# Kernel optimization log

Hardware: AMD Instinct MI355X
Metric: run time of the kernel (lower is better)

The kernel has to match this reference:

```python
import jax, jax.numpy as jnp
import numpy as np
from functools import partial

NUM_CLASSES = 4
HEAD_OUTS = [4, 2, 1, 3, 2, 2]  # class, offset, z, size, yaw, vel -> sum 14
VOXEL = (0.1, 0.1)
PC_RANGE = (0.0, -39.68, -3.0, 100.0, 39.68, 1.0)
MIN_RADIUS = 2.0
BN_EPS = 1e-5


def setup_inputs() -> dict:
    key = jax.random.key(0)
    ks = jax.random.split(key, 12)
    B, C, H, W, N = 4, 256, 200, 200, 128
    spatial_features = jax.random.normal(ks[0], (B, C, H, W), jnp.float32)
    # gt boxes: x,y,z,w,l,h,yaw,cls,vx,vy ; coords chosen so grid idx in [0,200)
    x = jax.random.uniform(ks[1], (B, N), jnp.float32, 0.5, 19.5)
    y = jax.random.uniform(ks[2], (B, N), jnp.float32, -39.0, -20.0)
    z = jax.random.uniform(ks[3], (B, N), jnp.float32, -2.0, 0.0)
    dims = jax.random.uniform(ks[4], (B, N, 3), jnp.float32, 1.0, 4.0)
    yaw = jax.random.uniform(ks[5], (B, N), jnp.float32, -3.14159, 3.14159)
    cls = jax.random.randint(ks[6], (B, N), 0, NUM_CLASSES).astype(jnp.float32)
    vel = 0.1 * jax.random.normal(ks[7], (B, N, 2), jnp.float32)
    gt = jnp.concatenate([x[..., None], y[..., None], z[..., None], dims,
                          yaw[..., None], cls[..., None], vel], axis=-1)
    # zero out last 16 boxes per sample -> filtered by validity mask
    gt = gt.at[:, -16:, :].set(0.0)
    w1 = 0.05 * jax.random.normal(ks[8], (6, C, C, 3, 3), jnp.float32)
    bn_gamma = jnp.ones((6, C), jnp.float32)
    bn_beta = jnp.zeros((6, C), jnp.float32)
    bn_mean = 0.1 * jax.random.normal(ks[9], (6, C), jnp.float32)
    bn_var = jax.random.uniform(ks[10], (6, C), jnp.float32, 0.5, 1.5)
    w2 = 0.05 * jax.random.normal(ks[11], (14, C, 1, 1), jnp.float32)
    b2 = jnp.zeros((14,), jnp.float32)
    return {"spatial_features": spatial_features, "gt_boxes": gt, "w1": w1,
            "bn_gamma": bn_gamma, "bn_beta": bn_beta, "bn_mean": bn_mean,
            "bn_var": bn_var, "w2": w2, "b2": b2}


def _conv(x, w, pad):
    return jax.lax.conv_general_dilated(x, w, (1, 1), pad,
                                        dimension_numbers=("NCHW", "OIHW", "NCHW"))


def _heads(x, w1, g, b, m, v, w2, b2):
    outs, o = [], 0
    for i, nout in enumerate(HEAD_OUTS):
        h = _conv(x, w1[i], "SAME")  # [B,C,H,W]
        h = g[i][None, :, None, None] * (h - m[i][None, :, None, None]) \
            * jax.lax.rsqrt(v[i][None, :, None, None] + BN_EPS) + b[i][None, :, None, None]
        h = jax.nn.relu(h)
        outs.append(_conv(h, w2[o:o + nout], "VALID") + b2[o:o + nout][None, :, None, None])
        o += nout
    return jnp.concatenate(outs, axis=1)  # [B,14,H,W]


def _targets(gt, H, W):
    B, N = gt.shape[:2]
    x, y, z = gt[..., 0], gt[..., 1], gt[..., 2]
    bw, bl, bh = gt[..., 3], gt[..., 4], gt[..., 5]
    yaw = gt[..., 6]
    cls = jnp.clip(gt[..., 7].astype(jnp.int32), 0, NUM_CLASSES - 1)
    vel = gt[..., 8:10]
    valid = (jnp.abs(x) + jnp.abs(y) + jnp.abs(z)) > 0
    gx = (x - PC_RANGE[0]) / VOXEL[0]
    gy = (y - PC_RANGE[1]) / VOXEL[1]
    gxi = jnp.floor(gx).astype(jnp.int32)
    gyi = jnp.floor(gy).astype(jnp.int32)
    valid = valid & (gxi >= 0) & (gxi < W) & (gyi >= 0) & (gyi < H)
    xoff = gx - gxi.astype(gx.dtype)
    yoff = gy - gyi.astype(gy.dtype)
    # scalar targets scatter (invalid boxes dropped via out-of-range flat index)
    vals = jnp.stack([xoff, yoff, z, bw, bl, bh, jnp.sin(yaw), jnp.cos(yaw),
                      vel[..., 0], vel[..., 1], jnp.ones_like(x)], axis=-1)  # [B,N,11]
    bidx = jnp.broadcast_to(jnp.arange(B, dtype=jnp.int32)[:, None], (B, N))
    flat = bidx * (H * W) + gyi * W + gxi
    flat = jnp.where(valid, flat, B * H * W)  # out of range -> dropped
    scat = jnp.zeros((B * H * W, 11), jnp.float32)
    scat = scat.at[flat.reshape(-1)].set(vals.reshape(-1, 11), mode="drop")
    scalars = scat.reshape(B, H, W, 11).transpose(0, 3, 1, 2)  # [B,11,H,W]
    # gaussian heatmap: per-box splat, scatter-max into class channel
    sigma = jnp.maximum(jnp.sqrt(bw ** 2 + bl ** 2) / 2.0, MIN_RADIUS) / 3.0  # [B,N]
    xs = jnp.arange(W, dtype=jnp.float32)
    ys = jnp.arange(H, dtype=jnp.float32)
    d2 = (xs[None, None, None, :] - gxi[..., None, None].astype(jnp.float32)) ** 2 + \
         (ys[None, None, :, None] - gyi[..., None, None].astype(jnp.float32)) ** 2  # [B,N,H,W]
    gauss = jnp.exp(-d2 / (2.0 * sigma[..., None, None] ** 2))
    gauss = jnp.where(valid[..., None, None], gauss, 0.0)
    heat = jnp.zeros((B, NUM_CLASSES, H, W), jnp.float32)
    heat = heat.at[bidx, cls].max(gauss)
    return jnp.concatenate([heat, scalars], axis=1)  # [B,15,H,W]


def reference(spatial_features, gt_boxes, w1, bn_gamma, bn_beta, bn_mean, bn_var, w2, b2):
    H, W = spatial_features.shape[-2:]
    preds = _heads(spatial_features, w1, bn_gamma, bn_beta, bn_mean, bn_var, w2, b2)
    tgts = _targets(gt_boxes, H, W)
    return jnp.concatenate([preds, tgts], axis=1)  # [B,29,H,W]
```

## Files before the change

kernel.cpp:

```cpp
#include <hip/hip_runtime.h>

typedef __attribute__((ext_vector_type(8))) short short8;
typedef __attribute__((ext_vector_type(4))) float f32x4;
typedef __attribute__((ext_vector_type(4))) unsigned short us4;
typedef __attribute__((ext_vector_type(8))) unsigned short us8;

union FragU { short8 s; us4 h[2]; us8 u; };

__device__ __forceinline__ unsigned short f2bf(float f) {
  union { float f; unsigned int u; } v; v.f = f;
  unsigned int r = (v.u + 0x7fffu + ((v.u >> 16) & 1u)) >> 16;
  return (unsigned short)r;
}

__global__ void transpose_k(const float* __restrict__ sf, unsigned short* __restrict__ Xt) {
  __shared__ float tile[32][33];
  int b = blockIdx.z, c0 = blockIdx.y * 32, p0 = blockIdx.x * 32;
  int tx = threadIdx.x, ty = threadIdx.y;
#pragma unroll
  for (int i = 0; i < 4; ++i)
    tile[ty + i * 8][tx] = sf[((size_t)(b * 256 + c0 + ty + i * 8) * 40000) + p0 + tx];
  __syncthreads();
#pragma unroll
  for (int i = 0; i < 4; ++i)
    Xt[((size_t)(b * 40000 + p0 + ty + i * 8) << 8) + c0 + tx] = f2bf(tile[tx][ty + i * 8]);
}

__global__ void prep_w1f_k(const float* __restrict__ w1, const float* __restrict__ gamma,
                           const float* __restrict__ var, unsigned short* __restrict__ W1f) {
  int id = blockIdx.x * 256 + threadIdx.x;
  if (id >= 6 * 256 * 2304) return;
  int k = id % 2304;
  int rest = id / 2304;
  int oc = rest & 255, h = rest >> 8;
  int tap = k >> 8, c = k & 255;
  int hc = h * 256 + oc;
  float s = gamma[hc] * rsqrtf(var[hc] + 1e-5f);
  W1f[id] = f2bf(s * w1[(hc * 256 + c) * 9 + tap]);
}

__global__ __launch_bounds__(512) void conv_head_xt_k(
    const unsigned short* __restrict__ Xt, const unsigned short* __restrict__ W1f,
    const float* __restrict__ gamma, const float* __restrict__ beta,
    const float* __restrict__ mean, const float* __restrict__ var,
    const float* __restrict__ w2, const float* __restrict__ b2,
    float* __restrict__ out) {
  const int NOUT[6] = {4, 2, 1, 3, 2, 2};
  const int OFFS[6] = {0, 4, 6, 7, 10, 12};
  __shared__ __align__(16) char smem[78080];
  unsigned short* A_s  = (unsigned short*)smem;
  unsigned short* B_s  = (unsigned short*)(smem + 9216);
  unsigned short* h_s  = (unsigned short*)smem;
  unsigned short* w2_s = (unsigned short*)(smem + 67584);
  float* tb_s          = (float*)(smem + 76032);

  int tid = threadIdx.x;
  int head = blockIdx.z, b = blockIdx.y;
  int p_loc = blockIdx.x * 128;
  int nout = NOUT[head], ooff = OFFS[head];

  {
    int j = tid >> 5, c8 = (tid & 31) * 8;
    us8 t;
#pragma unroll
    for (int q = 0; q < 8; ++q)
      t[q] = (j < nout) ? f2bf(w2[(ooff + j) * 256 + c8 + q]) : (unsigned short)0;
    *(us8*)&w2_s[j * 264 + c8] = t;
  }
  if (tid < 256) {
    int hc = head * 256 + tid;
    float s = gamma[hc] * rsqrtf(var[hc] + 1e-5f);
    tb_s[tid] = beta[hc] - s * mean[hc];
  }
  __syncthreads();

  int wid = tid >> 6, lane = tid & 63;
  int wm = wid >> 2, wn = wid & 3;
  int l15 = lane & 15, lhi = lane >> 4;

  int apx = tid >> 2, cofs = (tid & 3) << 3;
  int pA = p_loc + apx;
  int aay = pA / 200, aax = pA - aay * 200;
  const unsigned short* xb = Xt + ((size_t)b * 40000 << 8);

  int oc = tid >> 1, half = tid & 1;
  const unsigned short* wsrc = W1f + (size_t)(head * 256 + oc) * 2304 + half * 16;

  f32x4 acc[4][4];
#pragma unroll
  for (int mi = 0; mi < 4; ++mi)
#pragma unroll
    for (int ni = 0; ni < 4; ++ni) acc[mi][ni] = (f32x4){0.f, 0.f, 0.f, 0.f};

  us8 aN, b0N, b1N;
  {
    int yy = aay - 1, xx = aax - 1;
    aN = (us8){0, 0, 0, 0, 0, 0, 0, 0};
    if ((unsigned)yy < 200u && (unsigned)xx < 200u)
      aN = *(const us8*)&xb[((size_t)(yy * 200 + xx) << 8) + cofs];
    b0N = *(const us8*)(wsrc);
    b1N = *(const us8*)(wsrc + 8);
  }

  for (int kt = 0; kt < 72; ++kt) {
    {
      FragU ua; ua.u = aN;
      int ao = apx * 36 + cofs;
      *(us4*)&A_s[ao] = ua.h[0];
      *(us4*)&A_s[ao + 4] = ua.h[1];
      FragU u0, u1; u0.u = b0N; u1.u = b1N;
      int bo = oc * 36 + half * 16;
      *(us4*)&B_s[bo]      = u0.h[0];
      *(us4*)&B_s[bo + 4]  = u0.h[1];
      *(us4*)&B_s[bo + 8]  = u1.h[0];
      *(us4*)&B_s[bo + 12] = u1.h[1];
    }
    __syncthreads();

    if (kt < 71) {
      int kn = kt + 1;
      int tap = kn >> 3, c0 = (kn & 7) << 5;
      int t3 = tap / 3;
      int dy = t3 - 1, dx = tap - t3 * 3 - 1;
      int yy = aay + dy, xx = aax + dx;
      aN = (us8){0, 0, 0, 0, 0, 0, 0, 0};
      if ((unsigned)yy < 200u && (unsigned)xx < 200u)
        aN = *(const us8*)&xb[((size_t)(yy * 200 + xx) << 8) + c0 + cofs];
      b0N = *(const us8*)(wsrc + kn * 32);
      b1N = *(const us8*)(wsrc + kn * 32 + 8);
    }

    short8 af[4], bfr[4];
#pragma unroll
    for (int mi = 0; mi < 4; ++mi) {
      int a = (wm * 64 + mi * 16 + l15) * 36 + lhi * 8;
      FragU u;
      u.h[0] = *(const us4*)&A_s[a];
      u.h[1] = *(const us4*)&A_s[a + 4];
      af[mi] = u.s;
    }
#pragma unroll
    for (int ni = 0; ni < 4; ++ni) {
      int a = (wn * 64 + ni * 16 + l15) * 36 + lhi * 8;
      FragU u;
      u.h[0] = *(const us4*)&B_s[a];
      u.h[1] = *(const us4*)&B_s[a + 4];
      bfr[ni] = u.s;
    }
#pragma unroll
    for (int mi = 0; mi < 4; ++mi)
#pragma unroll
      for (int ni = 0; ni < 4; ++ni)
        acc[mi][ni] = __builtin_amdgcn_mfma_f32_16x16x32_bf16(af[mi], bfr[ni], acc[mi][ni], 0, 0, 0);
    __syncthreads();
  }

#pragma unroll
  for (int mi = 0; mi < 4; ++mi) {
#pragma unroll
    for (int ni = 0; ni < 4; ++ni) {
      int ocl = wn * 64 + ni * 16 + l15;
      float tbv = tb_s[ocl];
#pragma unroll
      for (int r = 0; r < 4; ++r) {
        int px = wm * 64 + mi * 16 + lhi * 4 + r;
        float v = fmaxf(acc[mi][ni][r] + tbv, 0.f);
        h_s[px * 264 + ocl] = f2bf(v);
      }
    }
  }
  __syncthreads();

  {
    int j = l15;
    float b2v = (j < nout) ? b2[ooff + j] : 0.f;
    f32x4 oacc = (f32x4){0.f, 0.f, 0.f, 0.f};
#pragma unroll
    for (int kc = 0; kc < 8; ++kc) {
      int koff = kc * 32 + lhi * 8;
      FragU hu, wu;
      hu.u = *(const us8*)&h_s[(wid * 16 + l15) * 264 + koff];
      wu.u = *(const us8*)&w2_s[l15 * 264 + koff];
      oacc = __builtin_amdgcn_mfma_f32_16x16x32_bf16(hu.s, wu.s, oacc, 0, 0, 0);
    }
    if (j < nout) {
      float* dst = out + (size_t)(b * 29 + ooff + j) * 40000;
#pragma unroll
      for (int r = 0; r < 4; ++r) {
        int px_g = p_loc + wid * 16 + lhi * 4 + r;
        if (px_g < 40000) dst[px_g] = oacc[r] + b2v;
      }
    }
  }
}

template <int BMODE>
__global__ __launch_bounds__(512) void conv_head_mfma_k(
    const float* __restrict__ sf, const unsigned short* __restrict__ W1f,
    const float* __restrict__ w1, const float* __restrict__ gamma,
    const float* __restrict__ beta, const float* __restrict__ mean,
    const float* __restrict__ var, const float* __restrict__ w2,
    const float* __restrict__ b2, float* __restrict__ out) {
  const int NOUT[6] = {4, 2, 1, 3, 2, 2};
  const int OFFS[6] = {0, 4, 6, 7, 10, 12};
  __shared__ __align__(16) char smem[78080];
  unsigned short* A_s  = (unsigned short*)smem;
  unsigned short* B_s  = (unsigned short*)(smem + 9216);
  unsigned short* h_s  = (unsigned short*)smem;
  unsigned short* w2_s = (unsigned short*)(smem + 67584);
  float* tb_s          = (float*)(smem + 76032);
  float* s_s           = (float*)(smem + 77056);

  int tid = threadIdx.x;
  int head = blockIdx.z, b = blockIdx.y;
  int p_loc = blockIdx.x * 128;
  int nout = NOUT[head], ooff = OFFS[head];
  {
    int j = tid >> 5, c8 = (tid & 31) * 8;
    us8 t;
#pragma unroll
    for (int q = 0; q < 8; ++q)
      t[q] = (j < nout) ? f2bf(w2[(ooff + j) * 256 + c8 + q]) : (unsigned short)0;
    *(us8*)&w2_s[j * 264 + c8] = t;
  }
  if (tid < 256) {
    int hc = head * 256 + tid;
    float s = gamma[hc] * rsqrtf(var[hc] + 1e-5f);
    s_s[tid] = s;
    tb_s[tid] = beta[hc] - s * mean[hc];
  }
  __syncthreads();

  int wid = tid >> 6, lane = tid & 63;
  int wm = wid >> 2, wn = wid & 3;
  int l15 = lane & 15, lhi = lane >> 4;
  int cg = wid, mm = lane;
  int p0 = p_loc + mm, p1 = p0 + 64;
  int ay0 = p0 / 200, ax0 = p0 - ay0 * 200;
  int ay1 = p1 / 200, ax1 = p1 - ay1 * 200;
  const float* sfb = sf + (size_t)b * 256 * 40000;
  int oc = tid >> 1, half = tid & 1;
  const unsigned short* wsrc = W1f + (size_t)(head * 256 + oc) * 2304 + half * 16;
  const float* w1h = w1 + ((size_t)head * 256 + oc) * 2304;
  float sv = s_s[oc];

  f32x4 acc[4][4];
#pragma unroll
  for (int mi = 0; mi < 4; ++mi)
#pragma unroll
    for (int ni = 0; ni < 4; ++ni) acc[mi][ni] = (f32x4){0.f, 0.f, 0.f, 0.f};

  for (int kt = 0; kt < 72; ++kt) {
    int tap = kt >> 3;
    int c0 = (kt & 7) << 5;
    int t3 = tap / 3;
    int dy = t3 - 1, dx = tap - t3 * 3 - 1;
    {
      const float* src = sfb + (size_t)(c0 + cg * 4) * 40000;
      int yy = ay0 + dy, xx = ax0 + dx;
      us4 v = (us4){0, 0, 0, 0};
      if ((unsigned)yy < 200u && (unsigned)xx < 200u) {
        int pix = yy * 200 + xx;
        v[0] = f2bf(src[pix]);
        v[1] = f2bf(src[40000 + pix]);
        v[2] = f2bf(src[80000 + pix]);
        v[3] = f2bf(src[120000 + pix]);
      }
      *(us4*)&A_s[mm * 36 + cg * 4] = v;
      yy = ay1 + dy; xx = ax1 + dx;
      us4 w = (us4){0, 0, 0, 0};
      if ((unsigned)yy < 200u && (unsigned)xx < 200u) {
        int pix = yy * 200 + xx;
        w[0] = f2bf(src[pix]);
        w[1] = f2bf(src[40000 + pix]);
        w[2] = f2bf(src[80000 + pix]);
        w[3] = f2bf(src[120000 + pix]);
      }
      *(us4*)&A_s[(mm + 64) * 36 + cg * 4] = w;
    }
    if (BMODE == 0) {
      FragU u0, u1;
      u0.u = *(const us8*)(wsrc + kt * 32);
      u1.u = *(const us8*)(wsrc + kt * 32 + 8);
      int bo = oc * 36 + half * 16;
      *(us4*)&B_s[bo]      = u0.h[0];
      *(us4*)&B_s[bo + 4]  = u0.h[1];
      *(us4*)&B_s[bo + 8]  = u1.h[0];
      *(us4*)&B_s[bo + 12] = u1.h[1];
    } else {
      int kk = half * 16;
#pragma unroll
      for (int g = 0; g < 4; ++g) {
        us4 t;
#pragma unroll
        for (int q = 0; q < 4; ++q)
          t[q] = f2bf(sv * w1h[(c0 + kk + g * 4 + q) * 9 + tap]);
        *(us4*)&B_s[oc * 36 + kk + g * 4] = t;
      }
    }
    __syncthreads();
    short8 af[4], bfr[4];
#pragma unroll
    for (int mi = 0; mi < 4; ++mi) {
      int a = (wm * 64 + mi * 16 + l15) * 36 + lhi * 8;
      FragU u;
      u.h[0] = *(const us4*)&A_s[a];
      u.h[1] = *(const us4*)&A_s[a + 4];
      af[mi] = u.s;
    }
#pragma unroll
    for (int ni = 0; ni < 4; ++ni) {
      int a = (wn * 64 + ni * 16 + l15) * 36 + lhi * 8;
      FragU u;
      u.h[0] = *(const us4*)&B_s[a];
      u.h[1] = *(const us4*)&B_s[a + 4];
      bfr[ni] = u.s;
    }
#pragma unroll
    for (int mi = 0; mi < 4; ++mi)
#pragma unroll
      for (int ni = 0; ni < 4; ++ni)
        acc[mi][ni] = __builtin_amdgcn_mfma_f32_16x16x32_bf16(af[mi], bfr[ni], acc[mi][ni], 0, 0, 0);
    __syncthreads();
  }
#pragma unroll
  for (int mi = 0; mi < 4; ++mi) {
#pragma unroll
    for (int ni = 0; ni < 4; ++ni) {
      int ocl = wn * 64 + ni * 16 + l15;
      float tbv = tb_s[ocl];
#pragma unroll
      for (int r = 0; r < 4; ++r) {
        int px = wm * 64 + mi * 16 + lhi * 4 + r;
        float v = fmaxf(acc[mi][ni][r] + tbv, 0.f);
        h_s[px * 264 + ocl] = f2bf(v);
      }
    }
  }
  __syncthreads();
  {
    int j = l15;
    float b2v = (j < nout) ? b2[ooff + j] : 0.f;
    f32x4 oacc = (f32x4){0.f, 0.f, 0.f, 0.f};
#pragma unroll
    for (int kc = 0; kc < 8; ++kc) {
      int koff = kc * 32 + lhi * 8;
      FragU hu, wu;
      hu.u = *(const us8*)&h_s[(wid * 16 + l15) * 264 + koff];
      wu.u = *(const us8*)&w2_s[l15 * 264 + koff];
      oacc = __builtin_amdgcn_mfma_f32_16x16x32_bf16(hu.s, wu.s, oacc, 0, 0, 0);
    }
    if (j < nout) {
      float* dst = out + (size_t)(b * 29 + ooff + j) * 40000;
#pragma unroll
      for (int r = 0; r < 4; ++r) {
        int px_g = p_loc + wid * 16 + lhi * 4 + r;
        if (px_g < 40000) dst[px_g] = oacc[r] + b2v;
      }
    }
  }
}

__global__ void heat_k(const float* __restrict__ gt, float* __restrict__ out) {
  __shared__ float bx[128], by[128], binv[128];
  __shared__ int bcls[128];
  int b = blockIdx.y, tid = threadIdx.x;
  if (tid < 128) {
    const float* g = gt + (b * 128 + tid) * 10;
    float x = g[0], y = g[1], z = g[2];
    bool valid = fabsf(x) + fabsf(y) + fabsf(z) > 0.f;
    float gx = x / 0.1f;
    float gy = (y + 39.68f) / 0.1f;
    float fx = floorf(gx), fy = floorf(gy);
    int gxi = (int)fx, gyi = (int)fy;
    valid = valid && gxi >= 0 && gxi < 200 && gyi >= 0 && gyi < 200;
    float bw = g[3], bl = g[4];
    float sigma = fmaxf(sqrtf(bw * bw + bl * bl) * 0.5f, 2.0f) / 3.0f;
    binv[tid] = valid ? 1.f / (2.f * sigma * sigma) : -1.f;
    bx[tid] = fx;
    by[tid] = fy;
    bcls[tid] = min(max((int)g[7], 0), 3);
  }
  __syncthreads();
  int pid = blockIdx.x * 256 + tid;
  if (pid >= 40000) return;
  float py = (float)(pid / 200);
  float px = (float)(pid - (pid / 200) * 200);
  float h0 = 0.f, h1 = 0.f, h2 = 0.f, h3 = 0.f;
  for (int n = 0; n < 128; ++n) {
    float inv = binv[n];
    if (inv < 0.f) continue;
    float ddx = px - bx[n], ddy = py - by[n];
    float t = (ddx * ddx + ddy * ddy) * inv;
    if (t > 40.f) continue;
    float e = __expf(-t);
    int c = bcls[n];
    h0 = fmaxf(h0, c == 0 ? e : 0.f);
    h1 = fmaxf(h1, c == 1 ? e : 0.f);
    h2 = fmaxf(h2, c == 2 ? e : 0.f);
    h3 = fmaxf(h3, c == 3 ? e : 0.f);
  }
  int base = (b * 29 + 14) * 40000 + pid;
  out[base] = h0;
  out[base + 40000] = h1;
  out[base + 80000] = h2;
  out[base + 120000] = h3;
#pragma unroll
  for (int q = 0; q < 11; ++q) out[base + (4 + q) * 40000] = 0.f;
}

__global__ void scatter_k(const float* __restrict__ gt, float* __restrict__ out) {
  int b = threadIdx.x;
  if (b >= 4) return;
  for (int n = 0; n < 128; ++n) {
    const float* g = gt + (b * 128 + n) * 10;
    float x = g[0], y = g[1], z = g[2];
    if (!(fabsf(x) + fabsf(y) + fabsf(z) > 0.f)) continue;
    float gx = x / 0.1f;
    float gy = (y + 39.68f) / 0.1f;
    float fx = floorf(gx), fy = floorf(gy);
    int gxi = (int)fx, gyi = (int)fy;
    if (gxi < 0 || gxi >= 200 || gyi < 0 || gyi >= 200) continue;
    int base = (b * 29 + 18) * 40000 + gyi * 200 + gxi;
    out[base] = gx - fx;
    out[base + 1 * 40000] = gy - fy;
    out[base + 2 * 40000] = z;
    out[base + 3 * 40000] = g[3];
    out[base + 4 * 40000] = g[4];
    out[base + 5 * 40000] = g[5];
    out[base + 6 * 40000] = sinf(g[6]);
    out[base + 7 * 40000] = cosf(g[6]);
    out[base + 8 * 40000] = g[8];
    out[base + 9 * 40000] = g[9];
    out[base + 10 * 40000] = 1.f;
  }
}

extern "C" void kernel_launch(void* const* d_in, const int* in_sizes, int n_in,
                              void* d_out, int out_size, void* d_ws, size_t ws_size,
                              hipStream_t stream) {
  const float* sf    = (const float*)d_in[0];
  const float* gt    = (const float*)d_in[1];
  const float* w1    = (const float*)d_in[2];
  const float* gamma = (const float*)d_in[3];
  const float* beta  = (const float*)d_in[4];
  const float* mean  = (const float*)d_in[5];
  const float* var   = (const float*)d_in[6];
  const float* w2    = (const float*)d_in[7];
  const float* b2    = (const float*)d_in[8];
  float* out = (float*)d_out;
  char* ws = (char*)d_ws;

  const size_t W1F_BYTES = (size_t)6 * 256 * 2304 * 2;
  const size_t XT_BYTES  = (size_t)4 * 40000 * 256 * 2;
  unsigned short* W1f = (unsigned short*)ws;
  unsigned short* Xt  = (unsigned short*)(ws + W1F_BYTES);

  dim3 cgrid(313, 4, 6);
  if (ws_size >= W1F_BYTES + XT_BYTES) {
    prep_w1f_k<<<(6 * 256 * 2304 + 255) / 256, 256, 0, stream>>>(w1, gamma, var, W1f);
    transpose_k<<<dim3(1250, 8, 4), dim3(32, 8), 0, stream>>>(sf, Xt);
    conv_head_xt_k<<<cgrid, 512, 0, stream>>>(Xt, W1f, gamma, beta, mean, var, w2, b2, out);
  } else if (ws_size >= W1F_BYTES) {
    prep_w1f_k<<<(6 * 256 * 2304 + 255) / 256, 256, 0, stream>>>(w1, gamma, var, W1f);
    conv_head_mfma_k<0><<<cgrid, 512, 0, stream>>>(sf, W1f, w1, gamma, beta, mean, var, w2, b2, out);
  } else {
    conv_head_mfma_k<1><<<cgrid, 512, 0, stream>>>(sf, (const unsigned short*)nullptr,
                                                   w1, gamma, beta, mean, var, w2, b2, out);
  }
  heat_k<<<dim3(157, 4), 256, 0, stream>>>(gt, out);
  scatter_k<<<1, 64, 0, stream>>>(gt, out);
}
```

Measured before the change: 1.373 ms.

## Add padded-halo input layout and double-buffered direct-to-LDS loads in conv head

Adds a transpose kernel that writes bf16 activations into a zero-padded (202x202) pixel-major buffer. The new conv kernel can then load im2col tiles with no bounds checks, using global_load_lds so data goes straight from global memory into double-buffered LDS. This removes the register round-trip and the second barrier each K-step, and overlaps the next tile's load with the MFMA work. In exchange it needs a larger workspace and a full memset of the padded buffer each call, and it drops the old LDS row padding, which risks bank conflicts.

After: 1.277 ms. 7.0% less time.

```diff
diff --git a/kernel.cpp b/kernel.cpp
--- a/kernel.cpp
+++ b/kernel.cpp
@@ -11,6 +11,29 @@
   union { float f; unsigned int u; } v; v.f = f;
   unsigned int r = (v.u + 0x7fffu + ((v.u >> 16) & 1u)) >> 16;
   return (unsigned short)r;
+}
+
+typedef const __attribute__((address_space(1))) unsigned int* gas1_t;
+typedef __attribute__((address_space(3))) unsigned int* las3_t;
+__device__ __forceinline__ void glds16(const void* g, void* l) {
+  __builtin_amdgcn_global_load_lds((gas1_t)g, (las3_t)l, 16, 0, 0);
+}
+
+__global__ void transpose_pad_k(const float* __restrict__ sf, unsigned short* __restrict__ Xtp) {
+  __shared__ float tile[32][33];
+  int b = blockIdx.z, c0 = blockIdx.y * 32, p0 = blockIdx.x * 32;
+  int tx = threadIdx.x, ty = threadIdx.y;
+#pragma unroll
+  for (int i = 0; i < 4; ++i)
+    tile[ty + i * 8][tx] = sf[((size_t)(b * 256 + c0 + ty + i * 8) * 40000) + p0 + tx];
+  __syncthreads();
+#pragma unroll
+  for (int i = 0; i < 4; ++i) {
+    int p = p0 + ty + i * 8;
+    int y = p / 200, x = p - y * 200;
+    size_t pf = (size_t)b * 40804 + (size_t)(y + 1) * 202 + (x + 1);
+    Xtp[(pf << 8) + c0 + tx] = f2bf(tile[tx][ty + i * 8]);
+  }
 }
 
 __global__ void transpose_k(const float* __restrict__ sf, unsigned short* __restrict__ Xt) {
@@ -37,6 +60,140 @@
   int hc = h * 256 + oc;
   float s = gamma[hc] * rsqrtf(var[hc] + 1e-5f);
   W1f[id] = f2bf(s * w1[(hc * 256 + c) * 9 + tap]);
+}
+
+__global__ __launch_bounds__(512) void conv_head_glds_k(
+    const unsigned short* __restrict__ Xtp, const unsigned short* __restrict__ W1f,
+    const float* __restrict__ gamma, const float* __restrict__ beta,
+    const float* __restrict__ mean, const float* __restrict__ var,
+    const float* __restrict__ w2, const float* __restrict__ b2,
+    float* __restrict__ out) {
+  const int NOUT[6] = {4, 2, 1, 3, 2, 2};
+  const int OFFS[6] = {0, 4, 6, 7, 10, 12};
+  __shared__ __align__(16) char smem[77056];
+  unsigned short* h_s  = (unsigned short*)smem;
+  unsigned short* w2_s = (unsigned short*)(smem + 67584);
+  float* tb_s          = (float*)(smem + 76032);
+
+  int tid = threadIdx.x;
+  int head = blockIdx.z, b = blockIdx.y;
+  int p_loc = blockIdx.x * 128;
+  int nout = NOUT[head], ooff = OFFS[head];
+
+  {
+    int j = tid >> 5, c8 = (tid & 31) * 8;
+    us8 t;
+#pragma unroll
+    for (int q = 0; q < 8; ++q)
+      t[q] = (j < nout) ? f2bf(w2[(ooff + j) * 256 + c8 + q]) : (unsigned short)0;
+    *(us8*)&w2_s[j * 264 + c8] = t;
+  }
+  if (tid < 256) {
+    int hc = head * 256 + tid;
+    float s = gamma[hc] * rsqrtf(var[hc] + 1e-5f);
+    tb_s[tid] = beta[hc] - s * mean[hc];
+  }
+
+  int wid = tid >> 6, lane = tid & 63;
+  int wm = wid >> 2, wn = wid & 3;
+  int l15 = lane & 15, lhi = lane >> 4;
+
+  int apx = tid >> 2, cofs = (tid & 3) << 3;
+  int pA = p_loc + apx;
+  int pAc = pA < 40000 ? pA : 39999;
+  int ayy = pAc / 200, axx = pAc - ayy * 200;
+  int aflat = (ayy + 1) * 202 + (axx + 1);
+  const unsigned short* xbp = Xtp + (((size_t)b * 40804) << 8);
+
+  const unsigned short* bG0 = W1f + (size_t)(head * 256 + wid * 32 + (lane >> 2)) * 2304 + (lane & 3) * 8;
+  const unsigned short* bG1 = bG0 + 16 * 2304;
+
+  char* AL[2] = {smem + wid * 1024, smem + 24576 + wid * 1024};
+  char* BL[2] = {smem + 8192 + wid * 2048, smem + 32768 + wid * 2048};
+
+  f32x4 acc[4][4];
+#pragma unroll
+  for (int mi = 0; mi < 4; ++mi)
+#pragma unroll
+    for (int ni = 0; ni < 4; ++ni) acc[mi][ni] = (f32x4){0.f, 0.f, 0.f, 0.f};
+
+  glds16(xbp + (((size_t)(aflat - 203)) << 8) + cofs, AL[0]);
+  glds16(bG0, BL[0]);
+  glds16(bG1, BL[0] + 1024);
+  __syncthreads();
+
+  for (int kt = 0; kt < 72; ++kt) {
+    int cur = kt & 1;
+    if (kt < 71) {
+      int kn = kt + 1;
+      int tap = kn >> 3, c0 = (kn & 7) << 5;
+      int t3 = tap / 3;
+      int doff = (t3 - 1) * 202 + (tap - t3 * 3 - 1);
+      glds16(xbp + (((size_t)(aflat + doff)) << 8) + c0 + cofs, AL[cur ^ 1]);
+      glds16(bG0 + kn * 32, BL[cur ^ 1]);
+      glds16(bG1 + kn * 32, BL[cur ^ 1] + 1024);
+    }
+
+    const unsigned short* A_sh = (const unsigned short*)(smem + (cur ? 24576 : 0));
+    const unsigned short* B_sh = (const unsigned short*)(smem + (cur ? 32768 : 8192));
+    short8 af[4], bfr[4];
+#pragma unroll
+    for (int mi = 0; mi < 4; ++mi) {
+      FragU u;
+      u.u = *(const us8*)&A_sh[(wm * 64 + mi * 16 + l15) * 32 + lhi * 8];
+      af[mi] = u.s;
+    }
+#pragma unroll
+    for (int ni = 0; ni < 4; ++ni) {
+      FragU u;
+      u.u = *(const us8*)&B_sh[(wn * 64 + ni * 16 + l15) * 32 + lhi * 8];
+      bfr[ni] = u.s;
+    }
+#pragma unroll
+    for (int mi = 0; mi < 4; ++mi)
+#pragma unroll
+      for (int ni = 0; ni < 4; ++ni)
+        acc[mi][ni] = __builtin_amdgcn_mfma_f32_16x16x32_bf16(af[mi], bfr[ni], acc[mi][ni], 0, 0, 0);
+    __syncthreads();
+  }
+
+#pragma unroll
+  for (int mi = 0; mi < 4; ++mi) {
+#pragma unroll
+    for (int ni = 0; ni < 4; ++ni) {
+      int ocl = wn * 64 + ni * 16 + l15;
+      float tbv = tb_s[ocl];
+#pragma unroll
+      for (int r = 0; r < 4; ++r) {
+        int px = wm * 64 + mi * 16 + lhi * 4 + r;
+        float v = fmaxf(acc[mi][ni][r] + tbv, 0.f);
+        h_s[px * 264 + ocl] = f2bf(v);
+      }
+    }
+  }
+  __syncthreads();
+
+  {
+    int j = l15;
+    float b2v = (j < nout) ? b2[ooff + j] : 0.f;
+    f32x4 oacc = (f32x4){0.f, 0.f, 0.f, 0.f};
+#pragma unroll
+    for (int kc = 0; kc < 8; ++kc) {
+      int koff = kc * 32 + lhi * 8;
+      FragU hu, wu;
+      hu.u = *(const us8*)&h_s[(wid * 16 + l15) * 264 + koff];
+      wu.u = *(const us8*)&w2_s[l15 * 264 + koff];
+      oacc = __builtin_amdgcn_mfma_f32_16x16x32_bf16(hu.s, wu.s, oacc, 0, 0, 0);
+    }
+    if (j < nout) {
+      float* dst = out + (size_t)(b * 29 + ooff + j) * 40000;
+#pragma unroll
+      for (int r = 0; r < 4; ++r) {
+        int px_g = p_loc + wid * 16 + lhi * 4 + r;
+        if (px_g < 40000) dst[px_g] = oacc[r] + b2v;
+      }
+    }
+  }
 }
 
 __global__ __launch_bounds__(512) void conv_head_xt_k(
@@ -58,7 +215,6 @@
   int head = blockIdx.z, b = blockIdx.y;
   int p_loc = blockIdx.x * 128;
   int nout = NOUT[head], ooff = OFFS[head];
-
   {
     int j = tid >> 5, c8 = (tid & 31) * 8;
     us8 t;
@@ -77,12 +233,10 @@
   int wid = tid >> 6, lane = tid & 63;
   int wm = wid >> 2, wn = wid & 3;
   int l15 = lane & 15, lhi = lane >> 4;
-
   int apx = tid >> 2, cofs = (tid & 3) << 3;
   int pA = p_loc + apx;
   int aay = pA / 200, aax = pA - aay * 200;
   const unsigned short* xb = Xt + ((size_t)b * 40000 << 8);
-
   int oc = tid >> 1, half = tid & 1;
   const unsigned short* wsrc = W1f + (size_t)(head * 256 + oc) * 2304 + half * 16;
 
@@ -116,7 +270,6 @@
       *(us4*)&B_s[bo + 12] = u1.h[1];
     }
     __syncthreads();
-
     if (kt < 71) {
       int kn = kt + 1;
       int tap = kn >> 3, c0 = (kn & 7) << 5;
@@ -129,7 +282,6 @@
       b0N = *(const us8*)(wsrc + kn * 32);
       b1N = *(const us8*)(wsrc + kn * 32 + 8);
     }
-
     short8 af[4], bfr[4];
 #pragma unroll
     for (int mi = 0; mi < 4; ++mi) {
@@ -154,7 +306,6 @@
         acc[mi][ni] = __builtin_amdgcn_mfma_f32_16x16x32_bf16(af[mi], bfr[ni], acc[mi][ni], 0, 0, 0);
     __syncthreads();
   }
-
 #pragma unroll
   for (int mi = 0; mi < 4; ++mi) {
 #pragma unroll
@@ -170,7 +321,6 @@
     }
   }
   __syncthreads();
-
   {
     int j = l15;
     float b2v = (j < nout) ? b2[ooff + j] : 0.f;
@@ -194,13 +344,12 @@
   }
 }
 
-template <int BMODE>
-__global__ __launch_bounds__(512) void conv_head_mfma_k(
-    const float* __restrict__ sf, const unsigned short* __restrict__ W1f,
-    const float* __restrict__ w1, const float* __restrict__ gamma,
-    const float* __restrict__ beta, const float* __restrict__ mean,
-    const float* __restrict__ var, const float* __restrict__ w2,
-    const float* __restrict__ b2, float* __restrict__ out) {
+__global__ __launch_bounds__(512) void conv_head_nows_k(
+    const float* __restrict__ sf, const float* __restrict__ w1,
+    const float* __restrict__ gamma, const float* __restrict__ beta,
+    const float* __restrict__ mean, const float* __restrict__ var,
+    const float* __restrict__ w2, const float* __restrict__ b2,
+    float* __restrict__ out) {
   const int NOUT[6] = {4, 2, 1, 3, 2, 2};
   const int OFFS[6] = {0, 4, 6, 7, 10, 12};
   __shared__ __align__(16) char smem[78080];
@@ -240,7 +389,6 @@
   int ay1 = p1 / 200, ax1 = p1 - ay1 * 200;
   const float* sfb = sf + (size_t)b * 256 * 40000;
   int oc = tid >> 1, half = tid & 1;
-  const unsigned short* wsrc = W1f + (size_t)(head * 256 + oc) * 2304 + half * 16;
   const float* w1h = w1 + ((size_t)head * 256 + oc) * 2304;
   float sv = s_s[oc];
 
@@ -278,16 +426,7 @@
       }
       *(us4*)&A_s[(mm + 64) * 36 + cg * 4] = w;
     }
-    if (BMODE == 0) {
-      FragU u0, u1;
-      u0.u = *(const us8*)(wsrc + kt * 32);
-      u1.u = *(const us8*)(wsrc + kt * 32 + 8);
-      int bo = oc * 36 + half * 16;
-      *(us4*)&B_s[bo]      = u0.h[0];
-      *(us4*)&B_s[bo + 4]  = u0.h[1];
-      *(us4*)&B_s[bo + 8]  = u1.h[0];
-      *(us4*)&B_s[bo + 12] = u1.h[1];
-    } else {
+    {
       int kk = half * 16;
 #pragma unroll
       for (int g = 0; g < 4; ++g) {
@@ -453,20 +592,23 @@
 
   const size_t W1F_BYTES = (size_t)6 * 256 * 2304 * 2;
   const size_t XT_BYTES  = (size_t)4 * 40000 * 256 * 2;
+  const size_t XTP_BYTES = (size_t)4 * 40804 * 256 * 2;
   unsigned short* W1f = (unsigned short*)ws;
-  unsigned short* Xt  = (unsigned short*)(ws + W1F_BYTES);
 
   dim3 cgrid(313, 4, 6);
-  if (ws_size >= W1F_BYTES + XT_BYTES) {
+  if (ws_size >= W1F_BYTES + XTP_BYTES) {
+    unsigned short* Xtp = (unsigned short*)(ws + W1F_BYTES);
+    prep_w1f_k<<<(6 * 256 * 2304 + 255) / 256, 256, 0, stream>>>(w1, gamma, var, W1f);
+    hipMemsetAsync(Xtp, 0, XTP_BYTES, stream);
+    transpose_pad_k<<<dim3(1250, 8, 4), dim3(32, 8), 0, stream>>>(sf, Xtp);
+    conv_head_glds_k<<<cgrid, 512, 0, stream>>>(Xtp, W1f, gamma, beta, mean, var, w2, b2, out);
+  } else if (ws_size >= W1F_BYTES + XT_BYTES) {
+    unsigned short* Xt = (unsigned short*)(ws + W1F_BYTES);
     prep_w1f_k<<<(6 * 256 * 2304 + 255) / 256, 256, 0, stream>>>(w1, gamma, var, W1f);
     transpose_k<<<dim3(1250, 8, 4), dim3(32, 8), 0, stream>>>(sf, Xt);
     conv_head_xt_k<<<cgrid, 512, 0, stream>>>(Xt, W1f, gamma, beta, mean, var, w2, b2, out);
-  } else if (ws_size >= W1F_BYTES) {
-    prep_w1f_k<<<(6 * 256 * 2304 + 255) / 256, 256, 0, stream>>>(w1, gamma, var, W1f);
-    conv_head_mfma_k<0><<<cgrid, 512, 0, stream>>>(sf, W1f, w1, gamma, beta, mean, var, w2, b2, out);
   } else {
-    conv_head_mfma_k<1><<<cgrid, 512, 0, stream>>>(sf, (const unsigned short*)nullptr,
-                                                   w1, gamma, beta, mean, var, w2, b2, out);
+    conv_head_nows_k<<<cgrid, 512, 0, stream>>>(sf, w1, gamma, beta, mean, var, w2, b2, out);
   }
   heat_k<<<dim3(157, 4), 256, 0, stream>>>(gt, out);
   scatter_k<<<1, 64, 0, stream>>>(gt, out);
```

## Use zero-padded NHWC input and double-buffered direct-to-LDS loads in conv heads

Applied to the files above, without the earlier changes.

The transpose now writes into a zero-padded 202x202 bf16 NHWC buffer, so the conv kernel no longer needs boundary checks. The new conv kernel uses 256 threads with a 4x8 MFMA tile per wave and global_load_lds to copy A and B tiles straight into double-buffered shared memory, overlapping the next K-step's loads with the current MFMAs. The aim is to remove register staging, the extra barrier and the branchy loads. In exchange it adds a memset of the padded buffer, needs more accumulator registers, and drops the weight-only fallback path.

New measurement: 1.293 ms. 5.8% less time.

```diff
diff --git a/kernel.cpp b/kernel.cpp
--- a/kernel.cpp
+++ b/kernel.cpp
@@ -13,7 +13,13 @@
   return (unsigned short)r;
 }
 
-__global__ void transpose_k(const float* __restrict__ sf, unsigned short* __restrict__ Xt) {
+typedef const __attribute__((address_space(1))) unsigned int* gas1_t;
+typedef __attribute__((address_space(3))) unsigned int* las3_t;
+__device__ __forceinline__ void glds16(const void* g, void* l) {
+  __builtin_amdgcn_global_load_lds((gas1_t)g, (las3_t)l, 16, 0, 0);
+}
+
+__global__ void transpose_pad_k(const float* __restrict__ sf, unsigned short* __restrict__ Xtp) {
   __shared__ float tile[32][33];
   int b = blockIdx.z, c0 = blockIdx.y * 32, p0 = blockIdx.x * 32;
   int tx = threadIdx.x, ty = threadIdx.y;
@@ -22,8 +28,12 @@
     tile[ty + i * 8][tx] = sf[((size_t)(b * 256 + c0 + ty + i * 8) * 40000) + p0 + tx];
   __syncthreads();
 #pragma unroll
-  for (int i = 0; i < 4; ++i)
-    Xt[((size_t)(b * 40000 + p0 + ty + i * 8) << 8) + c0 + tx] = f2bf(tile[tx][ty + i * 8]);
+  for (int i = 0; i < 4; ++i) {
+    int p = p0 + ty + i * 8;
+    int y = p / 200, x = p - y * 200;
+    size_t pf = (size_t)b * 40804 + (size_t)(y + 1) * 202 + (x + 1);
+    Xtp[(pf << 8) + c0 + tx] = f2bf(tile[tx][ty + i * 8]);
+  }
 }
 
 __global__ void prep_w1f_k(const float* __restrict__ w1, const float* __restrict__ gamma,
@@ -39,8 +49,170 @@
   W1f[id] = f2bf(s * w1[(hc * 256 + c) * 9 + tap]);
 }
 
-__global__ __launch_bounds__(512) void conv_head_xt_k(
-    const unsigned short* __restrict__ Xt, const unsigned short* __restrict__ W1f,
+__global__ __launch_bounds__(256, 2) void conv_head_v4_k(
+    const unsigned short* __restrict__ Xtp, const unsigned short* __restrict__ W1f,
+    const float* __restrict__ gamma, const float* __restrict__ beta,
+    const float* __restrict__ mean, const float* __restrict__ var,
+    const float* __restrict__ w2, const float* __restrict__ b2,
+    float* __restrict__ out) {
+  const int NOUT[6] = {4, 2, 1, 3, 2, 2};
+  const int OFFS[6] = {0, 4, 6, 7, 10, 12};
+  __shared__ __align__(16) char smem[76032];
+  unsigned short* h_s  = (unsigned short*)smem;
+  unsigned short* w2_s = (unsigned short*)(smem + 67584);
+
+  int tid = threadIdx.x;
+  int head = blockIdx.z, b = blockIdx.y;
+  int p_loc = blockIdx.x * 128;
+  int nout = NOUT[head], ooff = OFFS[head];
+
+  int wid = tid >> 6, lane = tid & 63;
+  int wm = wid >> 1, wn = wid & 1;
+  int l15 = lane & 15, lhi = lane >> 4;
+
+  {
+    int j = tid >> 4, cb = (tid & 15) * 16;
+    us8 t0, t1;
+#pragma unroll
+    for (int q = 0; q < 8; ++q) {
+      t0[q] = (j < nout) ? f2bf(w2[(ooff + j) * 256 + cb + q]) : (unsigned short)0;
+      t1[q] = (j < nout) ? f2bf(w2[(ooff + j) * 256 + cb + 8 + q]) : (unsigned short)0;
+    }
+    *(us8*)&w2_s[j * 264 + cb] = t0;
+    *(us8*)&w2_s[j * 264 + cb + 8] = t1;
+  }
+
+  int r0 = tid >> 2;
+  int cb16 = (tid & 3) * 16;
+  int pA0 = p_loc + r0;       if (pA0 > 39999) pA0 = 39999;
+  int pA1 = p_loc + r0 + 64;  if (pA1 > 39999) pA1 = 39999;
+  int ay0 = pA0 / 200, ax0 = pA0 - ay0 * 200;
+  int ay1 = pA1 / 200, ax1 = pA1 - ay1 * 200;
+  const char* xb = (const char*)Xtp + (size_t)b * 40804 * 512;
+  const char* As0 = xb + (size_t)((ay0 + 1) * 202 + ax0 + 1) * 512 + cb16;
+  const char* As1 = xb + (size_t)((ay1 + 1) * 202 + ax1 + 1) * 512 + cb16;
+
+  const char* Bs0 = (const char*)W1f + (size_t)(head * 256 + r0) * 4608 + cb16;
+  const char* Bs1 = Bs0 + (size_t)64 * 4608;
+  const char* Bs2 = Bs0 + (size_t)128 * 4608;
+  const char* Bs3 = Bs0 + (size_t)192 * 4608;
+
+  char* ALd[2] = {smem + wid * 1024, smem + 24576 + wid * 1024};
+  char* BLd[2] = {smem + 8192 + wid * 1024, smem + 32768 + wid * 1024};
+
+  f32x4 acc[4][8];
+#pragma unroll
+  for (int mi = 0; mi < 4; ++mi)
+#pragma unroll
+    for (int ni = 0; ni < 8; ++ni) acc[mi][ni] = (f32x4){0.f, 0.f, 0.f, 0.f};
+
+  {
+    long ab = -203L * 512;
+    glds16(As0 + ab, ALd[0]);
+    glds16(As1 + ab, ALd[0] + 4096);
+    glds16(Bs0, BLd[0]);
+    glds16(Bs1, BLd[0] + 4096);
+    glds16(Bs2, BLd[0] + 8192);
+    glds16(Bs3, BLd[0] + 12288);
+  }
+  __syncthreads();
+
+  for (int kt = 0; kt < 72; ++kt) {
+    int cur = kt & 1;
+    if (kt < 71) {
+      int kn = kt + 1;
+      int tap = kn >> 3;
+      int c0b = (kn & 7) << 6;
+      int t3 = tap / 3;
+      int doff = (t3 - 1) * 202 + (tap - t3 * 3 - 1);
+      long ab = (long)doff * 512 + c0b;
+      long bb = (long)kn * 64;
+      glds16(As0 + ab, ALd[cur ^ 1]);
+      glds16(As1 + ab, ALd[cur ^ 1] + 4096);
+      glds16(Bs0 + bb, BLd[cur ^ 1]);
+      glds16(Bs1 + bb, BLd[cur ^ 1] + 4096);
+      glds16(Bs2 + bb, BLd[cur ^ 1] + 8192);
+      glds16(Bs3 + bb, BLd[cur ^ 1] + 12288);
+    }
+    const unsigned short* A_sh = (const unsigned short*)(smem + (cur ? 24576 : 0));
+    const unsigned short* B_sh = (const unsigned short*)(smem + (cur ? 32768 : 8192));
+    short8 af[4], bfr[8];
+#pragma unroll
+    for (int mi = 0; mi < 4; ++mi) {
+      FragU u;
+      u.u = *(const us8*)&A_sh[(wm * 64 + mi * 16 + l15) * 32 + lhi * 8];
+      af[mi] = u.s;
+    }
+#pragma unroll
+    for (int ni = 0; ni < 8; ++ni) {
+      FragU u;
+      u.u = *(const us8*)&B_sh[(wn * 128 + ni * 16 + l15) * 32 + lhi * 8];
+      bfr[ni] = u.s;
+    }
+#pragma unroll
+    for (int mi = 0; mi < 4; ++mi)
+#pragma unroll
+      for (int ni = 0; ni < 8; ++ni)
+        acc[mi][ni] = __builtin_amdgcn_mfma_f32_16x16x32_bf16(af[mi], bfr[ni], acc[mi][ni], 0, 0, 0);
+    __syncthreads();
+  }
+
+  {
+    float tbr[8];
+#pragma unroll
+    for (int ni = 0; ni < 8; ++ni) {
+      int hc = head * 256 + wn * 128 + ni * 16 + l15;
+      float s = gamma[hc] * rsqrtf(var[hc] + 1e-5f);
+      tbr[ni] = beta[hc] - s * mean[hc];
+    }
+#pragma unroll
+    for (int mi = 0; mi < 4; ++mi)
+#pragma unroll
+      for (int ni = 0; ni < 8; ++ni)
+#pragma unroll
+        for (int r = 0; r < 4; ++r)
+          acc[mi][ni][r] = fmaxf(acc[mi][ni][r] + tbr[ni], 0.f);
+  }
+#pragma unroll
+  for (int mi = 0; mi < 4; ++mi) {
+#pragma unroll
+    for (int ni = 0; ni < 8; ++ni) {
+      int ocl = wn * 128 + ni * 16 + l15;
+#pragma unroll
+      for (int r = 0; r < 4; ++r) {
+        int px = wm * 64 + mi * 16 + lhi * 4 + r;
+        h_s[px * 264 + ocl] = f2bf(acc[mi][ni][r]);
+      }
+    }
+  }
+  __syncthreads();
+
+#pragma unroll
+  for (int g2 = 0; g2 < 2; ++g2) {
+    int grp = wid * 2 + g2;
+    float b2v = (l15 < nout) ? b2[ooff + l15] : 0.f;
+    f32x4 oacc = (f32x4){0.f, 0.f, 0.f, 0.f};
+#pragma unroll
+    for (int kc = 0; kc < 8; ++kc) {
+      int koff = kc * 32 + lhi * 8;
+      FragU hu, wu;
+      hu.u = *(const us8*)&h_s[(grp * 16 + l15) * 264 + koff];
+      wu.u = *(const us8*)&w2_s[l15 * 264 + koff];
+      oacc = __builtin_amdgcn_mfma_f32_16x16x32_bf16(hu.s, wu.s, oacc, 0, 0, 0);
+    }
+    if (l15 < nout) {
+      float* dst = out + (size_t)(b * 29 + ooff + l15) * 40000;
+#pragma unroll
+      for (int r = 0; r < 4; ++r) {
+        int px_g = p_loc + grp * 16 + lhi * 4 + r;
+        if (px_g < 40000) dst[px_g] = oacc[r] + b2v;
+      }
+    }
+  }
+}
+
+__global__ __launch_bounds__(512) void conv_head_nows_k(
+    const float* __restrict__ sf, const float* __restrict__ w1,
     const float* __restrict__ gamma, const float* __restrict__ beta,
     const float* __restrict__ mean, const float* __restrict__ var,
     const float* __restrict__ w2, const float* __restrict__ b2,
@@ -53,162 +225,6 @@
   unsigned short* h_s  = (unsigned short*)smem;
   unsigned short* w2_s = (unsigned short*)(smem + 67584);
   float* tb_s          = (float*)(smem + 76032);
-
-  int tid = threadIdx.x;
-  int head = blockIdx.z, b = blockIdx.y;
-  int p_loc = blockIdx.x * 128;
-  int nout = NOUT[head], ooff = OFFS[head];
-
-  {
-    int j = tid >> 5, c8 = (tid & 31) * 8;
-    us8 t;
-#pragma unroll
-    for (int q = 0; q < 8; ++q)
-      t[q] = (j < nout) ? f2bf(w2[(ooff + j) * 256 + c8 + q]) : (unsigned short)0;
-    *(us8*)&w2_s[j * 264 + c8] = t;
-  }
-  if (tid < 256) {
-    int hc = head * 256 + tid;
-    float s = gamma[hc] * rsqrtf(var[hc] + 1e-5f);
-    tb_s[tid] = beta[hc] - s * mean[hc];
-  }
-  __syncthreads();
-
-  int wid = tid >> 6, lane = tid & 63;
-  int wm = wid >> 2, wn = wid & 3;
-  int l15 = lane & 15, lhi = lane >> 4;
-
-  int apx = tid >> 2, cofs = (tid & 3) << 3;
-  int pA = p_loc + apx;
-  int aay = pA / 200, aax = pA - aay * 200;
-  const unsigned short* xb = Xt + ((size_t)b * 40000 << 8);
-
-  int oc = tid >> 1, half = tid & 1;
-  const unsigned short* wsrc = W1f + (size_t)(head * 256 + oc) * 2304 + half * 16;
-
-  f32x4 acc[4][4];
-#pragma unroll
-  for (int mi = 0; mi < 4; ++mi)
-#pragma unroll
-    for (int ni = 0; ni < 4; ++ni) acc[mi][ni] = (f32x4){0.f, 0.f, 0.f, 0.f};
-
-  us8 aN, b0N, b1N;
-  {
-    int yy = aay - 1, xx = aax - 1;
-    aN = (us8){0, 0, 0, 0, 0, 0, 0, 0};
-    if ((unsigned)yy < 200u && (unsigned)xx < 200u)
-      aN = *(const us8*)&xb[((size_t)(yy * 200 + xx) << 8) + cofs];
-    b0N = *(const us8*)(wsrc);
-    b1N = *(const us8*)(wsrc + 8);
-  }
-
-  for (int kt = 0; kt < 72; ++kt) {
-    {
-      FragU ua; ua.u = aN;
-      int ao = apx * 36 + cofs;
-      *(us4*)&A_s[ao] = ua.h[0];
-      *(us4*)&A_s[ao + 4] = ua.h[1];
-      FragU u0, u1; u0.u = b0N; u1.u = b1N;
-      int bo = oc * 36 + half * 16;
-      *(us4*)&B_s[bo]      = u0.h[0];
-      *(us4*)&B_s[bo + 4]  = u0.h[1];
-      *(us4*)&B_s[bo + 8]  = u1.h[0];
-      *(us4*)&B_s[bo + 12] = u1.h[1];
-    }
-    __syncthreads();
-
-    if (kt < 71) {
-      int kn = kt + 1;
-      int tap = kn >> 3, c0 = (kn & 7) << 5;
-      int t3 = tap / 3;
-      int dy = t3 - 1, dx = tap - t3 * 3 - 1;
-      int yy = aay + dy, xx = aax + dx;
-      aN = (us8){0, 0, 0, 0, 0, 0, 0, 0};
-      if ((unsigned)yy < 200u && (unsigned)xx < 200u)
-        aN = *(const us8*)&xb[((size_t)(yy * 200 + xx) << 8) + c0 + cofs];
-      b0N = *(const us8*)(wsrc + kn * 32);
-      b1N = *(const us8*)(wsrc + kn * 32 + 8);
-    }
-
-    short8 af[4], bfr[4];
-#pragma unroll
-    for (int mi = 0; mi < 4; ++mi) {
-      int a = (wm * 64 + mi * 16 + l15) * 36 + lhi * 8;
-      FragU u;
-      u.h[0] = *(const us4*)&A_s[a];
-      u.h[1] = *(const us4*)&A_s[a + 4];
-      af[mi] = u.s;
-    }
-#pragma unroll
-    for (int ni = 0; ni < 4; ++ni) {
-      int a = (wn * 64 + ni * 16 + l15) * 36 + lhi * 8;
-      FragU u;
-      u.h[0] = *(const us4*)&B_s[a];
-      u.h[1] = *(const us4*)&B_s[a + 4];
-      bfr[ni] = u.s;
-    }
-#pragma unroll
-    for (int mi = 0; mi < 4; ++mi)
-#pragma unroll
-      for (int ni = 0; ni < 4; ++ni)
-        acc[mi][ni] = __builtin_amdgcn_mfma_f32_16x16x32_bf16(af[mi], bfr[ni], acc[mi][ni], 0, 0, 0);
-    __syncthreads();
-  }
-
-#pragma unroll
-  for (int mi = 0; mi < 4; ++mi) {
-#pragma unroll
-    for (int ni = 0; ni < 4; ++ni) {
-      int ocl = wn * 64 + ni * 16 + l15;
-      float tbv = tb_s[ocl];
-#pragma unroll
-      for (int r = 0; r < 4; ++r) {
-        int px = wm * 64 + mi * 16 + lhi * 4 + r;
-        float v = fmaxf(acc[mi][ni][r] + tbv, 0.f);
-        h_s[px * 264 + ocl] = f2bf(v);
-      }
-    }
-  }
-  __syncthreads();
-
-  {
-    int j = l15;
-    float b2v = (j < nout) ? b2[ooff + j] : 0.f;
-    f32x4 oacc = (f32x4){0.f, 0.f, 0.f, 0.f};
-#pragma unroll
-    for (int kc = 0; kc < 8; ++kc) {
-      int koff = kc * 32 + lhi * 8;
-      FragU hu, wu;
-      hu.u = *(const us8*)&h_s[(wid * 16 + l15) * 264 + koff];
-      wu.u = *(const us8*)&w2_s[l15 * 264 + koff];
-      oacc = __builtin_amdgcn_mfma_f32_16x16x32_bf16(hu.s, wu.s, oacc, 0, 0, 0);
-    }
-    if (j < nout) {
-      float* dst = out + (size_t)(b * 29 + ooff + j) * 40000;
-#pragma unroll
-      for (int r = 0; r < 4; ++r) {
-        int px_g = p_loc + wid * 16 + lhi * 4 + r;
-        if (px_g < 40000) dst[px_g] = oacc[r] + b2v;
-      }
-    }
-  }
-}
-
-template <int BMODE>
-__global__ __launch_bounds__(512) void conv_head_mfma_k(
-    const float* __restrict__ sf, const unsigned short* __restrict__ W1f,
-    const float* __restrict__ w1, const float* __restrict__ gamma,
-    const float* __restrict__ beta, const float* __restrict__ mean,
-    const float* __restrict__ var, const float* __restrict__ w2,
-    const float* __restrict__ b2, float* __restrict__ out) {
-  const int NOUT[6] = {4, 2, 1, 3, 2, 2};
-  const int OFFS[6] = {0, 4, 6, 7, 10, 12};
-  __shared__ __align__(16) char smem[78080];
-  unsigned short* A_s  = (unsigned short*)smem;
-  unsigned short* B_s  = (unsigned short*)(smem + 9216);
-  unsigned short* h_s  = (unsigned short*)smem;
-  unsigned short* w2_s = (unsigned short*)(smem + 67584);
-  float* tb_s          = (float*)(smem + 76032);
   float* s_s           = (float*)(smem + 77056);
 
   int tid = threadIdx.x;
@@ -240,7 +256,6 @@
   int ay1 = p1 / 200, ax1 = p1 - ay1 * 200;
   const float* sfb = sf + (size_t)b * 256 * 40000;
   int oc = tid >> 1, half = tid & 1;
-  const unsigned short* wsrc = W1f + (size_t)(head * 256 + oc) * 2304 + half * 16;
   const float* w1h = w1 + ((size_t)head * 256 + oc) * 2304;
   float sv = s_s[oc];
 
@@ -278,16 +293,7 @@
       }
       *(us4*)&A_s[(mm + 64) * 36 + cg * 4] = w;
     }
-    if (BMODE == 0) {
-      FragU u0, u1;
-      u0.u = *(const us8*)(wsrc + kt * 32);
-      u1.u = *(const us8*)(wsrc + kt * 32 + 8);
-      int bo = oc * 36 + half * 16;
-      *(us4*)&B_s[bo]      = u0.h[0];
-      *(us4*)&B_s[bo + 4]  = u0.h[1];
-      *(us4*)&B_s[bo + 8]  = u1.h[0];
-      *(us4*)&B_s[bo + 12] = u1.h[1];
-    } else {
+    {
       int kk = half * 16;
 #pragma unroll
       for (int g = 0; g < 4; ++g) {
@@ -452,21 +458,18 @@
   char* ws = (char*)d_ws;
 
   const size_t W1F_BYTES = (size_t)6 * 256 * 2304 * 2;
-  const size_t XT_BYTES  = (size_t)4 * 40000 * 256 * 2;
+  const size_t XTP_BYTES = (size_t)4 * 40804 * 256 * 2;
   unsigned short* W1f = (unsigned short*)ws;
-  unsigned short* Xt  = (unsigned short*)(ws + W1F_BYTES);
 
   dim3 cgrid(313, 4, 6);
-  if (ws_size >= W1F_BYTES + XT_BYTES) {
+  if (ws_size >= W1F_BYTES + XTP_BYTES) {
+    unsigned short* Xtp = (unsigned short*)(ws + W1F_BYTES);
     prep_w1f_k<<<(6 * 256 * 2304 + 255) / 256, 256, 0, stream>>>(w1, gamma, var, W1f);
-    transpose_k<<<dim3(1250, 8, 4), dim3(32, 8), 0, stream>>>(sf, Xt);
-    conv_head_xt_k<<<cgrid, 512, 0, stream>>>(Xt, W1f, gamma, beta, mean, var, w2, b2, out);
-  } else if (ws_size >= W1F_BYTES) {
-    prep_w1f_k<<<(6 * 256 * 2304 + 255) / 256, 256, 0, stream>>>(w1, gamma, var, W1f);
-    conv_head_mfma_k<0><<<cgrid, 512, 0, stream>>>(sf, W1f, w1, gamma, beta, mean, var, w2, b2, out);
+    hipMemsetAsync(Xtp, 0, XTP_BYTES, stream);
+    transpose_pad_k<<<dim3(1250, 8, 4), dim3(32, 8), 0, stream>>>(sf, Xtp);
+    conv_head_v4_k<<<cgrid, 256, 0, stream>>>(Xtp, W1f, gamma, beta, mean, var, w2, b2, out);
   } else {
-    conv_head_mfma_k<1><<<cgrid, 512, 0, stream>>>(sf, (const unsigned short*)nullptr,
-                                                   w1, gamma, beta, mean, var, w2, b2, out);
+    conv_head_nows_k<<<cgrid, 512, 0, stream>>>(sf, w1, gamma, beta, mean, var, w2, b2, out);
   }
   heat_k<<<dim3(157, 4), 256, 0, stream>>>(gt, out);
   scatter_k<<<1, 64, 0, stream>>>(gt, out);
```
